# Optimization experiments

Measured on AMD Instinct MI355X. Metric: run time of the kernel, lower is better.

## Reference

```python
import jax, jax.numpy as jnp
import numpy as np
from jax import lax

T = 16          # timesteps
EPS = 1e-12     # torch F.normalize eps
DN = ('NCHW', 'OIHW', 'NCHW')

def conv2d(x, w, pad):
    return lax.conv_general_dilated(x, w, (1, 1), [(pad, pad), (pad, pad)],
                                    dimension_numbers=DN)

def setup_inputs() -> dict:
    key = jax.random.key(0)
    ks = jax.random.split(key, 7)
    B, C, H, W, K = 16, 512, 14, 14, 64
    return {
        'input_tensor': jax.random.normal(ks[0], (B * T, C, H, W), jnp.float32),
        'centers': jax.random.normal(ks[1], (K, C), jnp.float32) * 0.05,
        'share_w': jax.random.normal(ks[2], (K, C, 1, 1), jnp.float32) * 0.05,
        'share_b': jax.random.uniform(ks[3], (K,), jnp.float32),
        'U_z': jax.random.normal(ks[4], (K, K, 3, 3), jnp.float32) * 0.05,
        'U_r': jax.random.normal(ks[5], (K, K, 3, 3), jnp.float32) * 0.05,
        'U_h': jax.random.normal(ks[6], (K, K, 3, 3), jnp.float32) * 0.05,
    }

def reference(input_tensor, centers, share_w, share_b, U_z, U_r, U_h):
    NT, C, H, W = input_tensor.shape
    B = NT // T
    K = centers.shape[0]

    # soft-assignment pre-activation: 1x1 conv (SAME) -> [B*T, K, H, W]
    wxb = conv2d(input_tensor, share_w, 0) + share_b[None, :, None, None]
    wxb = wxb.reshape(B, T, K, H, W).transpose(1, 0, 2, 3, 4)  # [T,B,K,H,W]

    def gru_step(h, wxb_t):
        z = jax.nn.sigmoid(wxb_t + conv2d(h, U_z, 1))
        r = jax.nn.sigmoid(wxb_t + conv2d(h, U_r, 1))
        hh = jnp.tanh(wxb_t + conv2d(r * h, U_h, 1))
        h_new = (1.0 - z) * hh + z * h
        return h_new, h_new

    h0 = jnp.zeros((B, K, H, W), input_tensor.dtype)
    _, assign = lax.scan(gru_step, h0, wxb)            # [T,B,K,H,W]
    assign = assign.transpose(1, 0, 2, 3, 4).reshape(B * T, K, H * W)

    a_sum = assign.sum(-1, keepdims=True)              # [BT,K,1]
    a = a_sum * centers[None]                          # [BT,K,C]
    feats = input_tensor.reshape(B * T, C, H * W)
    x = jnp.einsum('nks,ncs->nkc', assign, feats)      # [BT,K,C]

    vlad = (x - a).reshape(B, T, K, C).sum(1)          # [B,K,C]
    vlad = vlad / jnp.maximum(jnp.linalg.norm(vlad, axis=2, keepdims=True), EPS)
    vlad = vlad.reshape(B, K * C)
    vlad = vlad / jnp.maximum(jnp.linalg.norm(vlad, axis=1, keepdims=True), EPS)
    return vlad
```

## Files before the change

kernel.cpp:

```cpp
#include <hip/hip_runtime.h>

#define Bc 16
#define Tc 16
#define Cc 512
#define Kc 64
#define Sc 196
#define KS (Kc*Sc)
#define BKS (Bc*Kc*Sc)
#define TBKS (Tc*BKS)
#define GFIN (16*64*512)
#define PART_N (8*GFIN)
#define PL 288
#define PLB (Kc*PL)

__device__ __forceinline__ float sigmoid_f(float x) { return 1.f / (1.f + __expf(-x)); }
__device__ __forceinline__ float tanh_f(float x) { return 1.f - 2.f / (__expf(2.f * x) + 1.f); }

__global__ __launch_bounds__(256) void k_transpose_w(const float* __restrict__ w, float* __restrict__ wt) {
    int idx = blockIdx.x * 256 + threadIdx.x;
    if (idx < Kc * Cc) {
        int k = idx & 63, c = idx >> 6;
        wt[idx] = w[k * Cc + c];
    }
}

__global__ __launch_bounds__(256) void k_conv1x1(const float* __restrict__ x, const float* __restrict__ wt,
                                                 const float* __restrict__ bias, float* __restrict__ wxb) {
    __shared__ float Xs[64][64];
    const int tid = threadIdx.x;
    const int gs0 = blockIdx.x * 64;
    const int kw = __builtin_amdgcn_readfirstlane((tid >> 6) << 4);
    const int lane = tid & 63;
    const int rbase = (tid >> 6) * 16;
    const int gs_c = gs0 + lane;
    const int n_c = gs_c / Sc, s_c = gs_c - n_c * Sc;
    const float* xcol = x + (size_t)n_c * (Cc * Sc) + s_c;

    float xr[16];
#pragma unroll
    for (int q = 0; q < 16; ++q) xr[q] = xcol[(size_t)(rbase + q) * Sc];
    float acc[16] = {};
    for (int c0 = 0; c0 < Cc; c0 += 64) {
        __syncthreads();
#pragma unroll
        for (int q = 0; q < 16; ++q) Xs[rbase + q][lane] = xr[q];
        __syncthreads();
        if (c0 + 64 < Cc) {
#pragma unroll
            for (int q = 0; q < 16; ++q) xr[q] = xcol[(size_t)(c0 + 64 + rbase + q) * Sc];
        }
#pragma unroll 8
        for (int cc = 0; cc < 64; ++cc) {
            const float xv = Xs[cc][lane];
            const float* wp = wt + (size_t)(c0 + cc) * Kc + kw;
#pragma unroll
            for (int i = 0; i < 16; ++i) acc[i] += wp[i] * xv;
        }
    }
    const int t = n_c & 15, bb = n_c >> 4;
    float* op = wxb + (((size_t)t * Bc + bb) * Kc + kw) * Sc + s_c;
#pragma unroll
    for (int i = 0; i < 16; ++i)
        op[(size_t)i * Sc] = acc[i] + bias[kw + i];
}

__global__ __launch_bounds__(64) void k_gru_t0(const float* __restrict__ wxb,
        float* __restrict__ hplane, float* __restrict__ rhplane, float* __restrict__ assign) {
    const int blk = blockIdx.x;
    const size_t pbase = (size_t)blk * PL;
    const size_t cbase = (size_t)blk * Sc;
    for (int i = threadIdx.x; i < PL; i += 64) {
        int y = i >> 4, xx = i & 15;
        float v = 0.f;
        if (y >= 2 && y <= 15 && xx >= 1 && xx <= 14) {
            int s = (y - 2) * 14 + (xx - 1);
            float pre = wxb[cbase + s];
            v = (1.f - sigmoid_f(pre)) * tanh_f(pre);
            assign[cbase + s] = v;
        }
        hplane[pbase + i] = v;
        rhplane[pbase + i] = 0.f;
    }
}

__global__ __launch_bounds__(512) void k_gru_gates(const float* __restrict__ hplane,
        const float* __restrict__ wxb_t, const float* __restrict__ Uz, const float* __restrict__ Ur,
        float* __restrict__ zb, float* __restrict__ rhplane) {
    extern __shared__ float lds[];
    float* P = lds;
    float* red = lds + PLB;
    const int b = blockIdx.x;
    const int k0 = blockIdx.y * 4;
    const int tid = threadIdx.x;
    const int wv = __builtin_amdgcn_readfirstlane(tid >> 6);
    const int lane = tid & 63;

    float preE[4]; bool validE[4]; size_t baseE[4]; int pxE[4], setE[4];
#pragma unroll
    for (int q = 0; q < 4; ++q) {
        const int o = tid + q * 512;
        setE[q] = o >> 8; pxE[q] = o & 255;
        const int yq = pxE[q] >> 4, xb = pxE[q] & 15;
        validE[q] = (yq >= 1 && yq <= 14 && xb >= 1 && xb <= 14);
        const int kk = setE[q] >> 1;
        const int s = (yq - 1) * 14 + (xb - 1);
        baseE[q] = ((size_t)b * Kc + k0 + kk) * Sc + (validE[q] ? s : 0);
        preE[q] = validE[q] ? wxb_t[baseE[q]] : 0.f;
    }
    {
        const float4* src = (const float4*)(hplane + (size_t)b * PLB);
        float4* dst = (float4*)P;
        for (int q = tid; q < PLB / 4; q += 512) dst[q] = src[q];
    }
    __syncthreads();

    const int yp = lane >> 2, xq = (lane & 3) << 2;
    const float* uzb = Uz + (size_t)k0 * 576 + wv * 72;
    const float* urb = Ur + (size_t)k0 * 576 + wv * 72;
    float acc[4][2][4] = {};
    const float* Pw = P + (size_t)(wv * 8) * PL + yp * 16 + xq;
#pragma unroll 2
    for (int ki8 = 0; ki8 < 8; ++ki8) {
        const float* pk = Pw + ki8 * PL;
#pragma unroll
        for (int dy = 0; dy < 3; ++dy) {
            const float* row = pk + dy * 16;
            float4 m = *(const float4*)row;
            float e0 = row[-1], e4 = row[4];
#pragma unroll
            for (int kk = 0; kk < 4; ++kk) {
                const float* wz = uzb + kk * 576 + ki8 * 9 + dy * 3;
                float c0 = wz[0], c1 = wz[1], c2 = wz[2];
                acc[kk][0][0] += c0*e0  + c1*m.x + c2*m.y;
                acc[kk][0][1] += c0*m.x + c1*m.y + c2*m.z;
                acc[kk][0][2] += c0*m.y + c1*m.z + c2*m.w;
                acc[kk][0][3] += c0*m.z + c1*m.w + c2*e4;
                const float* wr = urb + kk * 576 + ki8 * 9 + dy * 3;
                float d0 = wr[0], d1 = wr[1], d2 = wr[2];
                acc[kk][1][0] += d0*e0  + d1*m.x + d2*m.y;
                acc[kk][1][1] += d0*m.x + d1*m.y + d2*m.z;
                acc[kk][1][2] += d0*m.y + d1*m.z + d2*m.w;
                acc[kk][1][3] += d0*m.z + d1*m.w + d2*e4;
            }
        }
    }
    {
        float* rp = red + (size_t)wv * 2048 + lane * 4;
#pragma unroll
        for (int kk = 0; kk < 4; ++kk)
#pragma unroll
            for (int g = 0; g < 2; ++g)
                *(float4*)(rp + (kk * 2 + g) * 256) =
                    make_float4(acc[kk][g][0], acc[kk][g][1], acc[kk][g][2], acc[kk][g][3]);
    }
    __syncthreads();
#pragma unroll
    for (int q = 0; q < 4; ++q) {
        const float* rp = red + setE[q] * 256 + pxE[q];
        float s0 = 0.f;
#pragma unroll
        for (int w8 = 0; w8 < 8; ++w8) s0 += rp[(size_t)w8 * 2048];
        if (validE[q]) {
            float sv = sigmoid_f(preE[q] + s0);
            const int kk = setE[q] >> 1;
            const int k = k0 + kk;
            if ((setE[q] & 1) == 0) {
                zb[baseE[q]] = sv;
            } else {
                const int yq = pxE[q] >> 4, xb = pxE[q] & 15;
                float hv = P[(size_t)k * PL + (yq + 1) * 16 + xb];
                rhplane[(size_t)b * PLB + (size_t)k * PL + (yq + 1) * 16 + xb] = sv * hv;
            }
        }
    }
}

__global__ __launch_bounds__(512) void k_gru_out(const float* __restrict__ rhplane,
        const float* __restrict__ wxb_t, const float* __restrict__ Uh, const float* __restrict__ zb,
        float* __restrict__ hplane, float* __restrict__ assign_t) {
    extern __shared__ float lds[];
    float* P = lds;
    float* red = lds + PLB;
    const int b = blockIdx.x;
    const int k0 = blockIdx.y * 4;
    const int tid = threadIdx.x;
    const int wv = __builtin_amdgcn_readfirstlane(tid >> 6);
    const int lane = tid & 63;

    float preE[2], zvE[2], hpE[2]; bool validE[2]; size_t baseE[2], pposE[2]; int pxE[2], setE[2];
#pragma unroll
    for (int q = 0; q < 2; ++q) {
        const int o = tid + q * 512;
        setE[q] = o >> 8; pxE[q] = o & 255;
        const int yq = pxE[q] >> 4, xb = pxE[q] & 15;
        validE[q] = (yq >= 1 && yq <= 14 && xb >= 1 && xb <= 14);
        const int s = (yq - 1) * 14 + (xb - 1);
        const int k = k0 + setE[q];
        baseE[q] = ((size_t)b * Kc + k) * Sc + (validE[q] ? s : 0);
        pposE[q] = (size_t)b * PLB + (size_t)k * PL + (yq + 1) * 16 + xb;
        preE[q] = 0.f; zvE[q] = 0.f; hpE[q] = 0.f;
        if (validE[q]) {
            preE[q] = wxb_t[baseE[q]];
            zvE[q] = zb[baseE[q]];
            hpE[q] = hplane[pposE[q]];
        }
    }
    {
        const float4* src = (const float4*)(rhplane + (size_t)b * PLB);
        float4* dst = (float4*)P;
        for (int q = tid; q < PLB / 4; q += 512) dst[q] = src[q];
    }
    __syncthreads();

    const int yp = lane >> 2, xq = (lane & 3) << 2;
    const float* uhb = Uh + (size_t)k0 * 576 + wv * 72;
    float acc[4][4] = {};
    const float* Pw = P + (size_t)(wv * 8) * PL + yp * 16 + xq;
#pragma unroll 2
    for (int ki8 = 0; ki8 < 8; ++ki8) {
        const float* pk = Pw + ki8 * PL;
#pragma unroll
        for (int dy = 0; dy < 3; ++dy) {
            const float* row = pk + dy * 16;
            float4 m = *(const float4*)row;
            float e0 = row[-1], e4 = row[4];
#pragma unroll
            for (int kk = 0; kk < 4; ++kk) {
                const float* wh = uhb + kk * 576 + ki8 * 9 + dy * 3;
                float c0 = wh[0], c1 = wh[1], c2 = wh[2];
                acc[kk][0] += c0*e0  + c1*m.x + c2*m.y;
                acc[kk][1] += c0*m.x + c1*m.y + c2*m.z;
                acc[kk][2] += c0*m.y + c1*m.z + c2*m.w;
                acc[kk][3] += c0*m.z + c1*m.w + c2*e4;
            }
        }
    }
    {
        float* rp = red + (size_t)wv * 1024 + lane * 4;
#pragma unroll
        for (int kk = 0; kk < 4; ++kk)
            *(float4*)(rp + kk * 256) = make_float4(acc[kk][0], acc[kk][1], acc[kk][2], acc[kk][3]);
    }
    __syncthreads();
#pragma unroll
    for (int q = 0; q < 2; ++q) {
        const float* rp = red + setE[q] * 256 + pxE[q];
        float s0 = 0.f;
#pragma unroll
        for (int w8 = 0; w8 < 8; ++w8) s0 += rp[(size_t)w8 * 1024];
        if (validE[q]) {
            float hh = tanh_f(preE[q] + s0);
            float hn = (1.f - zvE[q]) * hh + zvE[q] * hpE[q];
            hplane[pposE[q]] = hn;
            assign_t[baseE[q]] = hn;
        }
    }
}

__global__ __launch_bounds__(256) void k_einsum(const float* __restrict__ x, const float* __restrict__ assign,
                                                float* __restrict__ part) {
    extern __shared__ float lds[];
    float* As = lds;
    float* Xs = lds + 196 * 68;
    const int ch = blockIdx.x, tg = blockIdx.y, b = blockIdx.z;
    const int tid = threadIdx.x;
    const int w = tid >> 6, lane = tid & 63;
    const int kt3 = lane >> 3, ct3 = lane & 7;
    const int kbase = kt3 * 8;
    const int cbase = w * 32 + ct3 * 4;
    float4 acc[8] = {};
    for (int tt = 0; tt < 2; ++tt) {
        const int t = tg * 2 + tt;
        const int n = b * Tc + t;
        __syncthreads();
        {
            const float* ap = assign + ((size_t)t * Bc + b) * KS;
            for (int q = tid; q < 3136; q += 256) {
                int kq = q / Sc, s = q - kq * Sc;
                int k4 = kq * 4;
                float4 v;
                v.x = ap[(size_t)(k4 + 0) * Sc + s];
                v.y = ap[(size_t)(k4 + 1) * Sc + s];
                v.z = ap[(size_t)(k4 + 2) * Sc + s];
                v.w = ap[(size_t)(k4 + 3) * Sc + s];
                *(float4*)(As + (size_t)s * 68 + k4) = v;
            }
        }
        for (int sc = 0; sc < 7; ++sc) {
            const int sb = sc * 28;
            __syncthreads();
            {
                const int c = tid & 127, sh = tid >> 7;
                const float* xp = x + ((size_t)n * Cc + ch * 128 + c) * Sc + sb + sh * 16;
                const int nf = sh ? 3 : 4;
                for (int f = 0; f < nf; ++f) {
                    float4 v = *(const float4*)(xp + f * 4);
                    float* dst = Xs + (size_t)(sh * 16 + f * 4) * 132 + c;
                    dst[0] = v.x; dst[132] = v.y; dst[264] = v.z; dst[396] = v.w;
                }
            }
            __syncthreads();
#pragma unroll 4
            for (int s = 0; s < 28; ++s) {
                const float* ap = As + (size_t)(sb + s) * 68 + kbase;
                float4 a0 = *(const float4*)ap;
                float4 a1 = *(const float4*)(ap + 4);
                float4 xv = *(const float4*)(Xs + (size_t)s * 132 + cbase);
                float av[8] = {a0.x,a0.y,a0.z,a0.w,a1.x,a1.y,a1.z,a1.w};
#pragma unroll
                for (int i = 0; i < 8; ++i) {
                    acc[i].x += av[i] * xv.x;
                    acc[i].y += av[i] * xv.y;
                    acc[i].z += av[i] * xv.z;
                    acc[i].w += av[i] * xv.w;
                }
            }
        }
    }
#pragma unroll
    for (int i = 0; i < 8; ++i) {
        const int k = kbase + i;
        float* op = part + (((size_t)tg * Bc + b) * Kc + k) * Cc + ch * 128 + cbase;
        *(float4*)op = acc[i];
    }
}

__global__ __launch_bounds__(256) void k_reduce(const float* __restrict__ assign, const float* __restrict__ part,
        const float* __restrict__ centers, float* __restrict__ vlad, float* __restrict__ norm2) {
    __shared__ float redw[4];
    __shared__ float a_s;
    const int blk = blockIdx.x;
    const int b = blk >> 6, k = blk & 63;
    const int tid = threadIdx.x;
    const int wave = tid >> 6, lane = tid & 63;
    const size_t bkoff = ((size_t)b * Kc + k) * Sc;
    float s = 0.f;
    for (int q = tid; q < 784; q += 256) {
        int t = q / 49, s4 = q - t * 49;
        float4 v = *(const float4*)(assign + (size_t)t * BKS + bkoff + s4 * 4);
        s += (v.x + v.y) + (v.z + v.w);
    }
#pragma unroll
    for (int o = 1; o < 64; o <<= 1) s += __shfl_xor(s, o);
    if (lane == 0) redw[wave] = s;
    __syncthreads();
    if (tid == 0) a_s = redw[0] + redw[1] + redw[2] + redw[3];
    __syncthreads();
    const float a = a_s;
    const size_t base = ((size_t)b * Kc + k) * Cc;
    const int c = tid * 2;
    float2 acc2 = make_float2(0.f, 0.f);
#pragma unroll
    for (int g = 0; g < 8; ++g) {
        float2 p = *(const float2*)(part + (size_t)g * GFIN + base + c);
        acc2.x += p.x; acc2.y += p.y;
    }
    float2 cv = *(const float2*)(centers + (size_t)k * Cc + c);
    float v0 = acc2.x - a * cv.x, v1 = acc2.y - a * cv.y;
    *(float2*)(vlad + base + c) = make_float2(v0, v1);
    float ss = v0 * v0 + v1 * v1;
#pragma unroll
    for (int o = 1; o < 64; o <<= 1) ss += __shfl_xor(ss, o);
    __syncthreads();
    if (lane == 0) redw[wave] = ss;
    __syncthreads();
    if (tid == 0) norm2[blk] = redw[0] + redw[1] + redw[2] + redw[3];
}

__global__ __launch_bounds__(64) void k_norms(const float* __restrict__ norm2, float* __restrict__ scl) {
    const int b = blockIdx.x;
    const int k = threadIdx.x;
    float ss = norm2[b * Kc + k];
    float inv = 1.f / fmaxf(sqrtf(ss), 1e-12f);
    float g = ss * inv * inv;
#pragma unroll
    for (int o = 1; o < 64; o <<= 1) g += __shfl_xor(g, o);
    float gi = 1.f / fmaxf(sqrtf(g), 1e-12f);
    scl[b * Kc + k] = inv * gi;
}

__global__ __launch_bounds__(256) void k_scale(const float* __restrict__ vlad, const float* __restrict__ scl,
                                               float* __restrict__ out) {
    const int blk = blockIdx.x;
    const int b = blk >> 4, kt = blk & 15;
    const int tid = threadIdx.x;
    const int kk = tid >> 6, lane = tid & 63;
    const int k = kt * 4 + kk;
    const float sv = scl[b * Kc + k];
    const float* vp = vlad + ((size_t)b * Kc + k) * Cc + lane * 8;
    float* op = out + ((size_t)b * Kc + k) * Cc + lane * 8;
    float4 v0 = *(const float4*)vp;
    float4 v1 = *(const float4*)(vp + 4);
    *(float4*)op = make_float4(v0.x * sv, v0.y * sv, v0.z * sv, v0.w * sv);
    *(float4*)(op + 4) = make_float4(v1.x * sv, v1.y * sv, v1.z * sv, v1.w * sv);
}

extern "C" void kernel_launch(void* const* d_in, const int* in_sizes, int n_in,
                              void* d_out, int out_size, void* d_ws, size_t ws_size,
                              hipStream_t stream) {
    (void)in_sizes; (void)n_in; (void)out_size; (void)ws_size;
    const float* x       = (const float*)d_in[0];
    const float* centers = (const float*)d_in[1];
    const float* share_w = (const float*)d_in[2];
    const float* share_b = (const float*)d_in[3];
    const float* Uz      = (const float*)d_in[4];
    const float* Ur      = (const float*)d_in[5];
    const float* Uh      = (const float*)d_in[6];
    float* out = (float*)d_out;
    float* ws  = (float*)d_ws;

    float* part    = ws;
    float* vlad    = ws;
    float* wxb     = ws;
    float* rhplane = ws + (size_t)TBKS;
    float* assign  = ws + (size_t)PART_N;
    float* zb      = assign + (size_t)TBKS;
    float* hplane  = zb + (size_t)BKS;
    float* wt      = hplane + (size_t)Bc * PLB;
    float* norm2   = wt + (size_t)Kc * Cc;
    float* scl     = norm2 + (size_t)Bc * Kc;

    const size_t gates_lds = (size_t)(PLB + 8 * 8 * 256) * 4;
    const size_t outk_lds  = (size_t)(PLB + 8 * 4 * 256) * 4;
    const size_t ein_lds   = (size_t)(196 * 68 + 28 * 132) * 4;

    k_transpose_w<<<dim3(128), 256, 0, stream>>>(share_w, wt);
    k_conv1x1<<<dim3(784), 256, 0, stream>>>(x, wt, share_b, wxb);
    k_gru_t0<<<dim3(1024), 64, 0, stream>>>(wxb, hplane, rhplane, assign);
    for (int t = 1; t < Tc; ++t) {
        k_gru_gates<<<dim3(16, 16), 512, gates_lds, stream>>>(hplane, wxb + (size_t)t * BKS,
                                                              Uz, Ur, zb, rhplane);
        k_gru_out<<<dim3(16, 16), 512, outk_lds, stream>>>(rhplane, wxb + (size_t)t * BKS,
                                                           Uh, zb, hplane, assign + (size_t)t * BKS);
    }
    k_einsum<<<dim3(4, 8, 16), 256, ein_lds, stream>>>(x, assign, part);
    k_reduce<<<dim3(Bc * Kc), 256, 0, stream>>>(assign, part, centers, vlad, norm2);
    k_norms<<<dim3(Bc), 64, 0, stream>>>(norm2, scl);
    k_scale<<<dim3(256), 256, 0, stream>>>(vlad, scl, out);
}
```

Measured before the change: 530.1 us.

## Split GRU conv kernels to one output channel per block with DPP halo shifts

The GRU gate and output kernels now handle one output channel per block instead of four, giving a 16x64 grid and four times as many blocks. The padded plane shrinks from 18 to 16 rows, and the left and right halo values come from DPP row shifts across lanes rather than extra LDS loads. LDS use per block drops, which should raise occupancy and parallelism in these latency-bound recurrent steps. In exchange, each block reloads the full hidden-state plane into LDS, so total plane traffic is four times higher.

```diff
diff --git a/kernel.cpp b/kernel.cpp
--- a/kernel.cpp
+++ b/kernel.cpp
@@ -10,11 +10,18 @@
 #define TBKS (Tc*BKS)
 #define GFIN (16*64*512)
 #define PART_N (8*GFIN)
-#define PL 288
-#define PLB (Kc*PL)
+#define PX 256
+#define PLB2 (Kc*PX)
 
 __device__ __forceinline__ float sigmoid_f(float x) { return 1.f / (1.f + __expf(-x)); }
 __device__ __forceinline__ float tanh_f(float x) { return 1.f - 2.f / (__expf(2.f * x) + 1.f); }
+
+__device__ __forceinline__ float dpp_prev(float v) {
+    return __int_as_float(__builtin_amdgcn_mov_dpp(__float_as_int(v), 0x111, 0xf, 0xf, true));
+}
+__device__ __forceinline__ float dpp_next(float v) {
+    return __int_as_float(__builtin_amdgcn_mov_dpp(__float_as_int(v), 0x101, 0xf, 0xf, true));
+}
 
 __global__ __launch_bounds__(256) void k_transpose_w(const float* __restrict__ w, float* __restrict__ wt) {
     int idx = blockIdx.x * 256 + threadIdx.x;
@@ -67,13 +74,13 @@
 __global__ __launch_bounds__(64) void k_gru_t0(const float* __restrict__ wxb,
         float* __restrict__ hplane, float* __restrict__ rhplane, float* __restrict__ assign) {
     const int blk = blockIdx.x;
-    const size_t pbase = (size_t)blk * PL;
+    const size_t pbase = (size_t)blk * PX;
     const size_t cbase = (size_t)blk * Sc;
-    for (int i = threadIdx.x; i < PL; i += 64) {
-        int y = i >> 4, xx = i & 15;
+    for (int i = threadIdx.x; i < PX; i += 64) {
+        int row = i >> 4, col = i & 15;
         float v = 0.f;
-        if (y >= 2 && y <= 15 && xx >= 1 && xx <= 14) {
-            int s = (y - 2) * 14 + (xx - 1);
+        if (row >= 1 && row <= 14 && col >= 1 && col <= 14) {
+            int s = (row - 1) * 14 + (col - 1);
             float pre = wxb[cbase + s];
             v = (1.f - sigmoid_f(pre)) * tanh_f(pre);
             assign[cbase + s] = v;
@@ -88,88 +95,75 @@
         float* __restrict__ zb, float* __restrict__ rhplane) {
     extern __shared__ float lds[];
     float* P = lds;
-    float* red = lds + PLB;
+    float* red = lds + PLB2;
     const int b = blockIdx.x;
-    const int k0 = blockIdx.y * 4;
+    const int k = blockIdx.y;
     const int tid = threadIdx.x;
     const int wv = __builtin_amdgcn_readfirstlane(tid >> 6);
     const int lane = tid & 63;
 
-    float preE[4]; bool validE[4]; size_t baseE[4]; int pxE[4], setE[4];
-#pragma unroll
-    for (int q = 0; q < 4; ++q) {
-        const int o = tid + q * 512;
-        setE[q] = o >> 8; pxE[q] = o & 255;
-        const int yq = pxE[q] >> 4, xb = pxE[q] & 15;
-        validE[q] = (yq >= 1 && yq <= 14 && xb >= 1 && xb <= 14);
-        const int kk = setE[q] >> 1;
-        const int s = (yq - 1) * 14 + (xb - 1);
-        baseE[q] = ((size_t)b * Kc + k0 + kk) * Sc + (validE[q] ? s : 0);
-        preE[q] = validE[q] ? wxb_t[baseE[q]] : 0.f;
-    }
+    const int setE = tid >> 8;
+    const int pxE = tid & 255;
+    const int rE = pxE >> 4, xbE = pxE & 15;
+    const bool valE = (rE >= 1 && rE <= 14 && xbE >= 1 && xbE <= 14);
+    const size_t cbase = ((size_t)b * Kc + k) * Sc;
+    const int sE = (rE - 1) * 14 + (xbE - 1);
+    const float preE = valE ? wxb_t[cbase + sE] : 0.f;
+
     {
-        const float4* src = (const float4*)(hplane + (size_t)b * PLB);
+        const float4* src = (const float4*)(hplane + (size_t)b * PLB2);
         float4* dst = (float4*)P;
-        for (int q = tid; q < PLB / 4; q += 512) dst[q] = src[q];
+#pragma unroll
+        for (int it = 0; it < 8; ++it) dst[it * 512 + tid] = src[it * 512 + tid];
     }
     __syncthreads();
 
     const int yp = lane >> 2, xq = (lane & 3) << 2;
-    const float* uzb = Uz + (size_t)k0 * 576 + wv * 72;
-    const float* urb = Ur + (size_t)k0 * 576 + wv * 72;
-    float acc[4][2][4] = {};
-    const float* Pw = P + (size_t)(wv * 8) * PL + yp * 16 + xq;
+    const int rowbase = (yp > 0) ? (yp - 1) : 0;
+    const float* uzb = Uz + (size_t)k * 576 + wv * 72;
+    const float* urb = Ur + (size_t)k * 576 + wv * 72;
+    float az[4] = {}, ar[4] = {};
+    const float* Pw = P + (size_t)(wv * 8) * PX + rowbase * 16 + xq;
 #pragma unroll 2
     for (int ki8 = 0; ki8 < 8; ++ki8) {
-        const float* pk = Pw + ki8 * PL;
+        const float* pk = Pw + ki8 * PX;
 #pragma unroll
         for (int dy = 0; dy < 3; ++dy) {
-            const float* row = pk + dy * 16;
-            float4 m = *(const float4*)row;
-            float e0 = row[-1], e4 = row[4];
-#pragma unroll
-            for (int kk = 0; kk < 4; ++kk) {
-                const float* wz = uzb + kk * 576 + ki8 * 9 + dy * 3;
-                float c0 = wz[0], c1 = wz[1], c2 = wz[2];
-                acc[kk][0][0] += c0*e0  + c1*m.x + c2*m.y;
-                acc[kk][0][1] += c0*m.x + c1*m.y + c2*m.z;
-                acc[kk][0][2] += c0*m.y + c1*m.z + c2*m.w;
-                acc[kk][0][3] += c0*m.z + c1*m.w + c2*e4;
-                const float* wr = urb + kk * 576 + ki8 * 9 + dy * 3;
-                float d0 = wr[0], d1 = wr[1], d2 = wr[2];
-                acc[kk][1][0] += d0*e0  + d1*m.x + d2*m.y;
-                acc[kk][1][1] += d0*m.x + d1*m.y + d2*m.z;
-                acc[kk][1][2] += d0*m.y + d1*m.z + d2*m.w;
-                acc[kk][1][3] += d0*m.z + d1*m.w + d2*e4;
-            }
+            float4 m = *(const float4*)(pk + dy * 16);
+            float e0 = dpp_prev(m.w);
+            float e4 = dpp_next(m.x);
+            const float* wz = uzb + ki8 * 9 + dy * 3;
+            float c0 = wz[0], c1 = wz[1], c2 = wz[2];
+            az[0] += c0*e0  + c1*m.x + c2*m.y;
+            az[1] += c0*m.x + c1*m.y + c2*m.z;
+            az[2] += c0*m.y + c1*m.z + c2*m.w;
+            az[3] += c0*m.z + c1*m.w + c2*e4;
+            const float* wr = urb + ki8 * 9 + dy * 3;
+            float d0 = wr[0], d1 = wr[1], d2 = wr[2];
+            ar[0] += d0*e0  + d1*m.x + d2*m.y;
+            ar[1] += d0*m.x + d1*m.y + d2*m.z;
+            ar[2] += d0*m.y + d1*m.z + d2*m.w;
+            ar[3] += d0*m.z + d1*m.w + d2*e4;
         }
     }
     {
-        float* rp = red + (size_t)wv * 2048 + lane * 4;
-#pragma unroll
-        for (int kk = 0; kk < 4; ++kk)
-#pragma unroll
-            for (int g = 0; g < 2; ++g)
-                *(float4*)(rp + (kk * 2 + g) * 256) =
-                    make_float4(acc[kk][g][0], acc[kk][g][1], acc[kk][g][2], acc[kk][g][3]);
-    }
-    __syncthreads();
-#pragma unroll
-    for (int q = 0; q < 4; ++q) {
-        const float* rp = red + setE[q] * 256 + pxE[q];
+        float* rp = red + (size_t)wv * 512 + lane * 4;
+        *(float4*)rp = make_float4(az[0], az[1], az[2], az[3]);
+        *(float4*)(rp + 256) = make_float4(ar[0], ar[1], ar[2], ar[3]);
+    }
+    __syncthreads();
+    {
+        const float* q = red + setE * 256 + pxE;
         float s0 = 0.f;
 #pragma unroll
-        for (int w8 = 0; w8 < 8; ++w8) s0 += rp[(size_t)w8 * 2048];
-        if (validE[q]) {
-            float sv = sigmoid_f(preE[q] + s0);
-            const int kk = setE[q] >> 1;
-            const int k = k0 + kk;
-            if ((setE[q] & 1) == 0) {
-                zb[baseE[q]] = sv;
+        for (int w8 = 0; w8 < 8; ++w8) s0 += q[(size_t)w8 * 512];
+        if (valE) {
+            float sv = sigmoid_f(preE + s0);
+            if (setE == 0) {
+                zb[cbase + sE] = sv;
             } else {
-                const int yq = pxE[q] >> 4, xb = pxE[q] & 15;
-                float hv = P[(size_t)k * PL + (yq + 1) * 16 + xb];
-                rhplane[(size_t)b * PLB + (size_t)k * PL + (yq + 1) * 16 + xb] = sv * hv;
+                float hv = P[(size_t)k * PX + pxE];
+                rhplane[(size_t)b * PLB2 + (size_t)k * PX + pxE] = sv * hv;
             }
         }
     }
@@ -180,79 +174,70 @@
         float* __restrict__ hplane, float* __restrict__ assign_t) {
     extern __shared__ float lds[];
     float* P = lds;
-    float* red = lds + PLB;
+    float* red = lds + PLB2;
     const int b = blockIdx.x;
-    const int k0 = blockIdx.y * 4;
+    const int k = blockIdx.y;
     const int tid = threadIdx.x;
     const int wv = __builtin_amdgcn_readfirstlane(tid >> 6);
     const int lane = tid & 63;
 
-    float preE[2], zvE[2], hpE[2]; bool validE[2]; size_t baseE[2], pposE[2]; int pxE[2], setE[2];
-#pragma unroll
-    for (int q = 0; q < 2; ++q) {
-        const int o = tid + q * 512;
-        setE[q] = o >> 8; pxE[q] = o & 255;
-        const int yq = pxE[q] >> 4, xb = pxE[q] & 15;
-        validE[q] = (yq >= 1 && yq <= 14 && xb >= 1 && xb <= 14);
-        const int s = (yq - 1) * 14 + (xb - 1);
-        const int k = k0 + setE[q];
-        baseE[q] = ((size_t)b * Kc + k) * Sc + (validE[q] ? s : 0);
-        pposE[q] = (size_t)b * PLB + (size_t)k * PL + (yq + 1) * 16 + xb;
-        preE[q] = 0.f; zvE[q] = 0.f; hpE[q] = 0.f;
-        if (validE[q]) {
-            preE[q] = wxb_t[baseE[q]];
-            zvE[q] = zb[baseE[q]];
-            hpE[q] = hplane[pposE[q]];
-        }
+    const bool epi = (tid < 256);
+    const int pxE = tid & 255;
+    const int rE = pxE >> 4, xbE = pxE & 15;
+    const bool valE = epi && (rE >= 1 && rE <= 14 && xbE >= 1 && xbE <= 14);
+    const size_t cbase = ((size_t)b * Kc + k) * Sc;
+    const size_t pbase = (size_t)b * PLB2 + (size_t)k * PX;
+    const int sE = (rE - 1) * 14 + (xbE - 1);
+    float preE = 0.f, zvE = 0.f, hpE = 0.f;
+    if (valE) {
+        preE = wxb_t[cbase + sE];
+        zvE = zb[cbase + sE];
+        hpE = hplane[pbase + pxE];
     }
     {
-        const float4* src = (const float4*)(rhplane + (size_t)b * PLB);
+        const float4* src = (const float4*)(rhplane + (size_t)b * PLB2);
         float4* dst = (float4*)P;
-        for (int q = tid; q < PLB / 4; q += 512) dst[q] = src[q];
+#pragma unroll
+        for (int it = 0; it < 8; ++it) dst[it * 512 + tid] = src[it * 512 + tid];
     }
     __syncthreads();
 
     const int yp = lane >> 2, xq = (lane & 3) << 2;
-    const float* uhb = Uh + (size_t)k0 * 576 + wv * 72;
-    float acc[4][4] = {};
-    const float* Pw = P + (size_t)(wv * 8) * PL + yp * 16 + xq;
+    const int rowbase = (yp > 0) ? (yp - 1) : 0;
+    const float* uhb = Uh + (size_t)k * 576 + wv * 72;
+    float ah[4] = {};
+    const float* Pw = P + (size_t)(wv * 8) * PX + rowbase * 16 + xq;
 #pragma unroll 2
     for (int ki8 = 0; ki8 < 8; ++ki8) {
-        const float* pk = Pw + ki8 * PL;
+        const float* pk = Pw + ki8 * PX;
 #pragma unroll
         for (int dy = 0; dy < 3; ++dy) {
-            const float* row = pk + dy * 16;
-            float4 m = *(const float4*)row;
-            float e0 = row[-1], e4 = row[4];
-#pragma unroll
-            for (int kk = 0; kk < 4; ++kk) {
-                const float* wh = uhb + kk * 576 + ki8 * 9 + dy * 3;
-                float c0 = wh[0], c1 = wh[1], c2 = wh[2];
-                acc[kk][0] += c0*e0  + c1*m.x + c2*m.y;
-                acc[kk][1] += c0*m.x + c1*m.y + c2*m.z;
-                acc[kk][2] += c0*m.y + c1*m.z + c2*m.w;
-                acc[kk][3] += c0*m.z + c1*m.w + c2*e4;
-            }
+            float4 m = *(const float4*)(pk + dy * 16);
+            float e0 = dpp_prev(m.w);
+            float e4 = dpp_next(m.x);
+            const float* wh = uhb + ki8 * 9 + dy * 3;
+            float c0 = wh[0], c1 = wh[1], c2 = wh[2];
+            ah[0] += c0*e0  + c1*m.x + c2*m.y;
+            ah[1] += c0*m.x + c1*m.y + c2*m.z;
+            ah[2] += c0*m.y + c1*m.z + c2*m.w;
+            ah[3] += c0*m.z + c1*m.w + c2*e4;
         }
     }
     {
-        float* rp = red + (size_t)wv * 1024 + lane * 4;
-#pragma unroll
-        for (int kk = 0; kk < 4; ++kk)
-            *(float4*)(rp + kk * 256) = make_float4(acc[kk][0], acc[kk][1], acc[kk][2], acc[kk][3]);
-    }
-    __syncthreads();
-#pragma unroll
-    for (int q = 0; q < 2; ++q) {
-        const float* rp = red + setE[q] * 256 + pxE[q];
+        float* rp = red + (size_t)wv * 256 + lane * 4;
+        *(float4*)rp = make_float4(ah[0], ah[1], ah[2], ah[3]);
+    }
+    __syncthreads();
+    if (epi) {
+        const float* q = red + pxE;
         float s0 = 0.f;
 #pragma unroll
-        for (int w8 = 0; w8 < 8; ++w8) s0 += rp[(size_t)w8 * 1024];
-        if (validE[q]) {
-            float hh = tanh_f(preE[q] + s0);
-            float hn = (1.f - zvE[q]) * hh + zvE[q] * hpE[q];
-            hplane[pposE[q]] = hn;
-            assign_t[baseE[q]] = hn;
+        for (int w8 = 0; w8 < 8; ++w8) s0 += q[(size_t)w8 * 256];
+        if (valE) {
+            float hh = tanh_f(preE + s0);
+            float hn = (1.f - zvE) * hh + zvE * hpE;
+            hplane[pbase + pxE] = hn;
+            assign_t[cbase + sE] = hn;
         }
     }
 }
@@ -416,21 +401,21 @@
     float* assign  = ws + (size_t)PART_N;
     float* zb      = assign + (size_t)TBKS;
     float* hplane  = zb + (size_t)BKS;
-    float* wt      = hplane + (size_t)Bc * PLB;
+    float* wt      = hplane + (size_t)Bc * PLB2;
     float* norm2   = wt + (size_t)Kc * Cc;
     float* scl     = norm2 + (size_t)Bc * Kc;
 
-    const size_t gates_lds = (size_t)(PLB + 8 * 8 * 256) * 4;
-    const size_t outk_lds  = (size_t)(PLB + 8 * 4 * 256) * 4;
+    const size_t gates_lds = (size_t)(PLB2 + 8 * 2 * 256) * 4;
+    const size_t outk_lds  = (size_t)(PLB2 + 8 * 256) * 4;
     const size_t ein_lds   = (size_t)(196 * 68 + 28 * 132) * 4;
 
     k_transpose_w<<<dim3(128), 256, 0, stream>>>(share_w, wt);
     k_conv1x1<<<dim3(784), 256, 0, stream>>>(x, wt, share_b, wxb);
     k_gru_t0<<<dim3(1024), 64, 0, stream>>>(wxb, hplane, rhplane, assign);
     for (int t = 1; t < Tc; ++t) {
-        k_gru_gates<<<dim3(16, 16), 512, gates_lds, stream>>>(hplane, wxb + (size_t)t * BKS,
+        k_gru_gates<<<dim3(16, 64), 512, gates_lds, stream>>>(hplane, wxb + (size_t)t * BKS,
                                                               Uz, Ur, zb, rhplane);
-        k_gru_out<<<dim3(16, 16), 512, outk_lds, stream>>>(rhplane, wxb + (size_t)t * BKS,
+        k_gru_out<<<dim3(16, 64), 512, outk_lds, stream>>>(rhplane, wxb + (size_t)t * BKS,
                                                            Uh, zb, hplane, assign + (size_t)t * BKS);
     }
     k_einsum<<<dim3(4, 8, 16), 256, ein_lds, stream>>>(x, assign, part);
```

Result: faster. 464.6 us (-12.3%).
